# Kernel optimization log

Measured on AMD Instinct MI355X. Metric: run time of the kernel, lower is better.

The kernel has to match this reference:

```python
import jax, jax.numpy as jnp
import numpy as np

D_MODEL = 1024
D_STATE = 16
D_FFN = 4096
D_INNER = 2 * D_MODEL
DT_RANK = D_MODEL // 16  # 64
K = 3  # conv kernel size
B_SZ = 2
L = 2048


def setup_inputs() -> dict:
    key = jax.random.key(0)
    ks = jax.random.split(key, 10)
    f = jnp.float32
    s = 0.02
    A_log = jnp.log(jnp.broadcast_to(jnp.arange(1, D_STATE + 1, dtype=f), (D_INNER, D_STATE)))
    return {
        "x": jax.random.normal(ks[0], (B_SZ, L, D_MODEL), f),
        "in_proj_w": jax.random.normal(ks[1], (2 * D_INNER, D_MODEL), f) * s,
        "conv_w": jax.random.normal(ks[2], (D_INNER, K), f) * s,
        "conv_b": jnp.zeros((D_INNER,), f),
        "x_proj_w": jax.random.normal(ks[3], (DT_RANK + 2 * D_STATE, D_INNER), f) * s,
        "dt_proj_w": jax.random.normal(ks[4], (D_INNER, DT_RANK), f) * s,
        "dt_proj_b": jnp.full((D_INNER,), -4.0, f),  # softplus -> small init dt
        "A_log": A_log,
        "Dp": jnp.ones((D_INNER,), f),
        "out_proj_w": jax.random.normal(ks[5], (D_MODEL, D_INNER), f) * s,
        "w1": jax.random.normal(ks[6], (D_FFN, D_MODEL), f) * s,
        "b1": jnp.zeros((D_FFN,), f),
        "w2": jax.random.normal(ks[7], (D_MODEL, D_FFN), f) * s,
        "b2": jnp.zeros((D_MODEL,), f),
    }


def _mamba(x, in_proj_w, conv_w, conv_b, x_proj_w, dt_proj_w, dt_proj_b, A_log, Dp, out_proj_w):
    # x: [B, L, d_model]
    xz = x @ in_proj_w.T                       # [B, L, 2*d_inner]
    xp, z = jnp.split(xz, 2, axis=-1)          # each [B, L, d_inner]
    # causal depthwise conv over time
    xc = jnp.swapaxes(xp, 1, 2)                # [B, d_inner, L]
    kern = conv_w[:, None, :]                  # [d_inner, 1, K]
    xc = jax.lax.conv_general_dilated(xc, kern, (1,), [(K - 1, 0)], feature_group_count=D_INNER)
    xp = jax.nn.silu(jnp.swapaxes(xc, 1, 2) + conv_b)  # [B, L, d_inner]
    # input-dependent dt, B, C
    dbc = xp @ x_proj_w.T                      # [B, L, dt_rank + 2*d_state]
    dt = jax.nn.softplus(dbc[..., :DT_RANK] @ dt_proj_w.T + dt_proj_b)  # [B, L, d_inner]
    Bm = dbc[..., DT_RANK:DT_RANK + D_STATE]   # [B, L, d_state]
    Cm = dbc[..., DT_RANK + D_STATE:]          # [B, L, d_state]
    A = -jnp.exp(A_log)                        # [d_inner, d_state]

    def step(h, t):
        dt_t, B_t, C_t, x_t = t                # [B,d_inner],[B,n],[B,n],[B,d_inner]
        h = jnp.exp(dt_t[:, :, None] * A) * h + dt_t[:, :, None] * B_t[:, None, :] * x_t[:, :, None]
        y = jnp.einsum('bdn,bn->bd', h, C_t)
        return h, y

    h0 = jnp.zeros((x.shape[0], D_INNER, D_STATE), x.dtype)
    ts = (jnp.swapaxes(dt, 0, 1), jnp.swapaxes(Bm, 0, 1), jnp.swapaxes(Cm, 0, 1), jnp.swapaxes(xp, 0, 1))
    h_final, ys = jax.lax.scan(step, h0, ts)
    y = jnp.swapaxes(ys, 0, 1) + xp * Dp       # [B, L, d_inner]
    y = y * jax.nn.silu(z)
    return y @ out_proj_w.T, h_final


def reference(x, in_proj_w, conv_w, conv_b, x_proj_w, dt_proj_w, dt_proj_b, A_log, Dp, out_proj_w, w1, b1, w2, b2):
    ssm_out, new_state = _mamba(x, in_proj_w, conv_w, conv_b, x_proj_w, dt_proj_w, dt_proj_b, A_log, Dp, out_proj_w)
    x = x + ssm_out
    h = jax.nn.gelu(x @ w1.T + b1, approximate=False)
    x = x + (h @ w2.T + b2)
    return (x, new_state)
```

## Files before the change

### kernel.cpp

```cpp
#include <hip/hip_runtime.h>
#include <hip/hip_bf16.h>
#include <math.h>

using bf16 = __hip_bfloat16;

typedef __attribute__((ext_vector_type(8))) short short8;
typedef __attribute__((ext_vector_type(4))) short shortx4;
typedef __attribute__((ext_vector_type(4))) float floatx4;

#define D_MODEL 1024
#define D_STATE 16
#define D_FFN   4096
#define D_INNER 2048
#define DT_RANK 64
#define BSZ     2
#define SEQ     2048
#define MROWS   (BSZ*SEQ)
#define NCHUNK  16
#define CLEN    (SEQ/NCHUNK)

static __device__ __forceinline__ float bf2f(bf16 v) { return __bfloat162float(v); }
static __device__ __forceinline__ short f2s(float f) {
    bf16 h = __float2bfloat16(f);
    return *reinterpret_cast<short*>(&h);
}
static __device__ __forceinline__ float sbf(short s) {
    union { short s; bf16 h; } u; u.s = s; return __bfloat162float(u.h);
}
static __device__ __forceinline__ float rd(const bf16* p)  { return bf2f(*p); }
static __device__ __forceinline__ float rd(const float* p) { return *p; }
static __device__ __forceinline__ void  wr(bf16* p, float v)  { *p = __float2bfloat16(v); }
static __device__ __forceinline__ void  wr(float* p, float v) { *p = v; }

static __device__ __forceinline__ void gload16(const bf16* g, bf16* l) {
    __builtin_amdgcn_global_load_lds(
        (const __attribute__((address_space(1))) void*)g,
        (__attribute__((address_space(3))) void*)l, 16, 0, 0);
}

#define BK 32

enum { ACT_NONE = 0, ACT_GELU = 1, ACT_SOFTPLUS = 2 };

template<int ACT, bool HAS_BIAS, bool HAS_RES, typename TR, typename TC>
__global__ __launch_bounds__(256)
void gemm_bt(const bf16* __restrict__ A, int lda,
             const bf16* __restrict__ W,
             TC* __restrict__ C, int ldc,
             const float* __restrict__ bias,
             const TR* __restrict__ resid, int ldr,
             int K)
{
    __shared__ __align__(16) bf16 As[128 * BK];
    __shared__ __align__(16) bf16 Bs[128 * BK];

    const int tid  = threadIdx.x;
    const int lane = tid & 63;
    const int wid  = tid >> 6;
    const int wm   = wid >> 1;
    const int wn   = wid & 1;
    const int quad = lane >> 4;
    const int lrow = lane & 15;

    const long m0 = (long)blockIdx.y * 128;
    const long n0 = (long)blockIdx.x * 128;

    const int rA = lane >> 2;
    const int kA = (lane & 3) * 8;
    const int q0 = wid * 2, q1 = wid * 2 + 1;

    const bf16* Ag0 = A + (m0 + q0 * 16 + rA) * (long)lda + kA;
    const bf16* Ag1 = A + (m0 + q1 * 16 + rA) * (long)lda + kA;
    const bf16* Wg0 = W + (n0 + q0 * 16 + rA) * (long)K + kA;
    const bf16* Wg1 = W + (n0 + q1 * 16 + rA) * (long)K + kA;
    bf16* AsL0 = As + q0 * 512;
    bf16* AsL1 = As + q1 * 512;
    bf16* BsL0 = Bs + q0 * 512;
    bf16* BsL1 = Bs + q1 * 512;

    floatx4 acc[4][4] = {};

    for (int k0 = 0; k0 < K; k0 += BK) {
        __syncthreads();
        gload16(Ag0 + k0, AsL0);
        gload16(Ag1 + k0, AsL1);
        gload16(Wg0 + k0, BsL0);
        gload16(Wg1 + k0, BsL1);
        __syncthreads();

        short8 af[4], bfv[4];
        #pragma unroll
        for (int i = 0; i < 4; i++)
            af[i] = *(const short8*)(As + (wm * 64 + i * 16 + lrow) * BK + quad * 8);
        #pragma unroll
        for (int j = 0; j < 4; j++)
            bfv[j] = *(const short8*)(Bs + (wn * 64 + j * 16 + lrow) * BK + quad * 8);
        #pragma unroll
        for (int i = 0; i < 4; i++)
            #pragma unroll
            for (int j = 0; j < 4; j++)
                acc[i][j] = __builtin_amdgcn_mfma_f32_16x16x32_bf16(af[i], bfv[j], acc[i][j], 0, 0, 0);
    }

    #pragma unroll
    for (int j = 0; j < 4; j++) {
        const long col = n0 + wn * 64 + j * 16 + lrow;
        float bv = HAS_BIAS ? bias[col] : 0.0f;
        #pragma unroll
        for (int i = 0; i < 4; i++) {
            #pragma unroll
            for (int r = 0; r < 4; r++) {
                const long row = m0 + wm * 64 + i * 16 + quad * 4 + r;
                float v = acc[i][j][r] + bv;
                if (ACT == ACT_GELU)     v = 0.5f * v * (1.0f + erff(v * 0.70710678118f));
                if (ACT == ACT_SOFTPLUS) v = (v > 20.0f) ? v : log1pf(__expf(v));
                if (HAS_RES) v += rd(resid + row * (long)ldr + col);
                wr(C + row * (long)ldc + col, v);
            }
        }
    }
}

__global__ __launch_bounds__(256)
void cvt_bf16(const float* __restrict__ src, bf16* __restrict__ dst)
{
    long i = (long)blockIdx.x * 256 + threadIdx.x;
    float4 a = *((const float4*)src + i * 2);
    float4 b = *((const float4*)src + i * 2 + 1);
    short8 r;
    r[0] = f2s(a.x); r[1] = f2s(a.y); r[2] = f2s(a.z); r[3] = f2s(a.w);
    r[4] = f2s(b.x); r[5] = f2s(b.y); r[6] = f2s(b.z); r[7] = f2s(b.w);
    *(short8*)(dst + i * 8) = r;
}

__global__ __launch_bounds__(256)
void conv_silu(const bf16* __restrict__ xpre, const float* __restrict__ cw,
               const float* __restrict__ cb, bf16* __restrict__ xp)
{
    long i = (long)blockIdx.x * 256 + threadIdx.x;
    int  d  = (int)(i & (D_INNER - 1));
    long bl = i >> 11;
    long l  = bl & (SEQ - 1);

    float w0 = cw[d * 3 + 0];
    float w1 = cw[d * 3 + 1];
    float w2 = cw[d * 3 + 2];
    float acc = cb[d] + w2 * bf2f(xpre[i]);
    if (l >= 1) acc += w1 * bf2f(xpre[i - D_INNER]);
    if (l >= 2) acc += w0 * bf2f(xpre[i - 2 * D_INNER]);
    float s = acc / (1.0f + __expf(-acc));
    xp[i] = __float2bfloat16(s);
}

__global__ __launch_bounds__(256)
void pad_xproj(const float* __restrict__ src, bf16* __restrict__ dst)
{
    int i = blockIdx.x * 256 + threadIdx.x;
    int row = i >> 11, col = i & 2047;
    dst[i] = (row < 96) ? __float2bfloat16(src[row * 2048 + col])
                        : __float2bfloat16(0.0f);
}

#define SROWS 16
#define SDB   64
#define SNB   (CLEN/SROWS)

__global__ __launch_bounds__(256)
void scan_part(const bf16* __restrict__ dt, const bf16* __restrict__ xp,
               const bf16* __restrict__ dbc, const float* __restrict__ Alog,
               float* __restrict__ Pbuf, float* __restrict__ Qbuf)
{
    __shared__ float2 Ap[2][SROWS][SDB];
    __shared__ float  Bp[2][SROWS][16];

    const int tid  = threadIdx.x;
    const int c    = blockIdx.x & (NCHUNK - 1);
    const int dgrp = (blockIdx.x >> 4) & 31;
    const int b    = blockIdx.x >> 9;
    const int d0   = dgrp * SDB;
    const long row0 = (long)b * SEQ + (long)c * CLEN;

    const int sl  = tid >> 4;
    const int sq  = tid & 15;
    const int sd4 = sq * 4;

    const int nt = tid & 3;
    const int dl = tid >> 2;
    const int n0 = nt * 4;
    const int d  = d0 + dl;

    const float4 Av = *(const float4*)(Alog + d * 16 + n0);
    float Ad[4] = { -__expf(Av.x), -__expf(Av.y), -__expf(Av.z), -__expf(Av.w) };

    float rdt[4], rdx[4], rB;
    auto ldb = [&](int bb) {
        long row = row0 + bb * SROWS + sl;
        shortx4 dv = *(const shortx4*)(dt + row * D_INNER + d0 + sd4);
        shortx4 xv = *(const shortx4*)(xp + row * D_INNER + d0 + sd4);
        #pragma unroll
        for (int k = 0; k < 4; k++) {
            float f = sbf(dv[k]);
            rdt[k] = f;
            rdx[k] = f * sbf(xv[k]);
        }
        rB = bf2f(dbc[row * 128 + 64 + sq]);
    };
    auto stb = [&](int bb) {
        int s = bb & 1;
        #pragma unroll
        for (int k = 0; k < 4; k++)
            Ap[s][sl][sd4 + k] = make_float2(rdt[k], rdx[k]);
        Bp[s][sl][sq] = rB;
    };

    float h[4] = {0.f, 0.f, 0.f, 0.f};
    float sdt = 0.f;

    ldb(0); stb(0);
    for (int bb = 0; bb < SNB; bb++) {
        if (bb + 1 < SNB) ldb(bb + 1);
        __syncthreads();
        const int s = bb & 1;
        #pragma unroll
        for (int l = 0; l < SROWS; l++) {
            float2  a  = Ap[s][l][dl];
            floatx4 Bq = *(const floatx4*)&Bp[s][l][n0];
            sdt += a.x;
            #pragma unroll
            for (int k = 0; k < 4; k++)
                h[k] = __expf(a.x * Ad[k]) * h[k] + a.y * Bq[k];
        }
        if (bb + 1 < SNB) stb(bb + 1);
    }

    const long base = ((long)(b * NCHUNK + c) * D_INNER + d) * 16 + n0;
    floatx4 P = { __expf(Ad[0] * sdt), __expf(Ad[1] * sdt),
                  __expf(Ad[2] * sdt), __expf(Ad[3] * sdt) };
    floatx4 Q = { h[0], h[1], h[2], h[3] };
    *(floatx4*)(Pbuf + base) = P;
    *(floatx4*)(Qbuf + base) = Q;
}

__global__ __launch_bounds__(256)
void scan_combine(const float* __restrict__ Pbuf, float* __restrict__ Qbuf,
                  float* __restrict__ state)
{
    long i = (long)blockIdx.x * 256 + threadIdx.x;
    int  n = (int)(i & 15);
    int  d = (int)((i >> 4) & (D_INNER - 1));
    int  b = (int)(i >> 15);
    float h = 0.0f;
    #pragma unroll
    for (int c = 0; c < NCHUNK; c++) {
        const long idx = ((long)(b * NCHUNK + c) * D_INNER + d) * 16 + n;
        float P = Pbuf[idx], Q = Qbuf[idx];
        Qbuf[idx] = h;
        h = P * h + Q;
    }
    state[((long)b * D_INNER + d) * 16 + n] = h;
}

__global__ __launch_bounds__(256)
void scan_final(const bf16* __restrict__ dt, bf16* __restrict__ xp,
                const bf16* __restrict__ dbc, const float* __restrict__ Alog,
                const bf16* __restrict__ z, const float* __restrict__ Dp,
                const float* __restrict__ Qbuf)
{
    __shared__ float2 Ap [2][SROWS][SDB];
    __shared__ float2 BCp[2][SROWS][16];
    __shared__ float2 GWp[2][SROWS][SDB];

    const int tid  = threadIdx.x;
    const int c    = blockIdx.x & (NCHUNK - 1);
    const int dgrp = (blockIdx.x >> 4) & 31;
    const int b    = blockIdx.x >> 9;
    const int d0   = dgrp * SDB;
    const long row0 = (long)b * SEQ + (long)c * CLEN;

    const int sl  = tid >> 4;
    const int sq  = tid & 15;
    const int sd4 = sq * 4;

    const int nt = tid & 3;
    const int dl = tid >> 2;
    const int n0 = nt * 4;
    const int d  = d0 + dl;

    const float4 Av = *(const float4*)(Alog + d * 16 + n0);
    float Ad[4] = { -__expf(Av.x), -__expf(Av.y), -__expf(Av.z), -__expf(Av.w) };
    const float4 Dv = *(const float4*)(Dp + d0 + sd4);
    const float Dk[4] = { Dv.x, Dv.y, Dv.z, Dv.w };

    float rdt[4], rdx[4], rg[4], rw[4], rB, rC;
    auto ldb = [&](int bb) {
        long row = row0 + bb * SROWS + sl;
        shortx4 dv = *(const shortx4*)(dt + row * D_INNER + d0 + sd4);
        shortx4 xv = *(const shortx4*)(xp + row * D_INNER + d0 + sd4);
        shortx4 zv = *(const shortx4*)(z  + row * D_INNER + d0 + sd4);
        #pragma unroll
        for (int k = 0; k < 4; k++) {
            float f  = sbf(dv[k]);
            float xf = sbf(xv[k]);
            float zf = sbf(zv[k]);
            float g  = zf / (1.0f + __expf(-zf));
            rdt[k] = f;
            rdx[k] = f * xf;
            rg[k]  = g;
            rw[k]  = xf * Dk[k] * g;
        }
        rB = bf2f(dbc[row * 128 + 64 + sq]);
        rC = bf2f(dbc[row * 128 + 80 + sq]);
    };
    auto stb = [&](int bb) {
        int s = bb & 1;
        #pragma unroll
        for (int k = 0; k < 4; k++) {
            Ap [s][sl][sd4 + k] = make_float2(rdt[k], rdx[k]);
            GWp[s][sl][sd4 + k] = make_float2(rg[k], rw[k]);
        }
        BCp[s][sl][sq] = make_float2(rB, rC);
    };

    float h[4];
    {
        const long base = ((long)(b * NCHUNK + c) * D_INNER + d) * 16 + n0;
        floatx4 q = *(const floatx4*)(Qbuf + base);
        h[0] = q[0]; h[1] = q[1]; h[2] = q[2]; h[3] = q[3];
    }

    ldb(0); stb(0);
    for (int bb = 0; bb < SNB; bb++) {
        if (bb + 1 < SNB) ldb(bb + 1);
        __syncthreads();
        const int s = bb & 1;
        #pragma unroll
        for (int l = 0; l < SROWS; l++) {
            float2  a   = Ap[s][l][dl];
            floatx4 bc0 = *(const floatx4*)&BCp[s][l][n0];
            floatx4 bc1 = *(const floatx4*)&BCp[s][l][n0 + 2];
            float yv;
            h[0] = __expf(a.x * Ad[0]) * h[0] + a.y * bc0[0];
            yv   = h[0] * bc0[1];
            h[1] = __expf(a.x * Ad[1]) * h[1] + a.y * bc0[2];
            yv  += h[1] * bc0[3];
            h[2] = __expf(a.x * Ad[2]) * h[2] + a.y * bc1[0];
            yv  += h[2] * bc1[1];
            h[3] = __expf(a.x * Ad[3]) * h[3] + a.y * bc1[2];
            yv  += h[3] * bc1[3];
            yv += __shfl_xor(yv, 1);
            yv += __shfl_xor(yv, 2);
            if (nt == 0) {
                float2 gw = GWp[s][l][dl];
                float out = yv * gw.x + gw.y;
                xp[(row0 + bb * SROWS + l) * (long)D_INNER + d0 + dl] =
                    __float2bfloat16(out);
            }
        }
        if (bb + 1 < SNB) stb(bb + 1);
    }
}

extern "C" void kernel_launch(void* const* d_in, const int* in_sizes, int n_in,
                              void* d_out, int out_size, void* d_ws, size_t ws_size,
                              hipStream_t stream)
{
    const float* x      = (const float*)d_in[0];
    const float* inw    = (const float*)d_in[1];
    const float* convw  = (const float*)d_in[2];
    const float* convb  = (const float*)d_in[3];
    const float* xprojw = (const float*)d_in[4];
    const float* dtw    = (const float*)d_in[5];
    const float* dtbias = (const float*)d_in[6];
    const float* Alog   = (const float*)d_in[7];
    const float* Dp     = (const float*)d_in[8];
    const float* outw   = (const float*)d_in[9];
    const float* w1     = (const float*)d_in[10];
    const float* b1     = (const float*)d_in[11];
    const float* w2     = (const float*)d_in[12];
    const float* b2     = (const float*)d_in[13];

    float* out0 = (float*)d_out;
    float* out1 = out0 + (long)MROWS * D_MODEL;

    bf16* buf0 = (bf16*)d_ws;
    bf16* buf1 = buf0 + (long)MROWS * D_INNER;
    bf16* buf2 = buf1 + (long)MROWS * D_INNER;
    bf16* dbc  = buf2 + (long)MROWS * D_INNER;
    bf16* wpad = dbc  + (long)MROWS * 128;
    bf16* W8   = wpad + 128 * 2048;

    float* Pbuf = (float*)d_out;
    float* Qbuf = Pbuf + (long)BSZ * NCHUNK * D_INNER * 16;
    bf16*  xbf  = (bf16*)((char*)d_out + 8 * 1024 * 1024);

    dim3 blk(256);

    cvt_bf16<<<dim3(2048), blk, 0, stream>>>(x, xbf);
    cvt_bf16<<<dim3(2048), blk, 0, stream>>>(inw, W8);
    pad_xproj<<<dim3(1024), blk, 0, stream>>>(xprojw, wpad);

    gemm_bt<ACT_NONE, false, false, float, bf16>
        <<<dim3(16, 32), blk, 0, stream>>>(
        xbf, D_MODEL, W8, buf0, D_INNER, nullptr, (const float*)nullptr, 0, D_MODEL);

    gemm_bt<ACT_NONE, false, false, float, bf16>
        <<<dim3(16, 32), blk, 0, stream>>>(
        xbf, D_MODEL, W8 + (long)D_INNER * D_MODEL, buf2, D_INNER,
        nullptr, (const float*)nullptr, 0, D_MODEL);

    conv_silu<<<dim3(32768), blk, 0, stream>>>(buf0, convw, convb, buf1);

    gemm_bt<ACT_NONE, false, false, float, bf16>
        <<<dim3(1, 32), blk, 0, stream>>>(
        buf1, D_INNER, wpad, dbc, 128, nullptr, (const float*)nullptr, 0, D_INNER);

    cvt_bf16<<<dim3(64), blk, 0, stream>>>(dtw, W8);
    gemm_bt<ACT_SOFTPLUS, true, false, float, bf16>
        <<<dim3(16, 32), blk, 0, stream>>>(
        dbc, 128, W8, buf0, D_INNER, dtbias, (const float*)nullptr, 0, DT_RANK);

    scan_part<<<dim3(BSZ * NCHUNK * (D_INNER / SDB)), blk, 0, stream>>>(
        buf0, buf1, dbc, Alog, Pbuf, Qbuf);
    scan_combine<<<dim3(256), blk, 0, stream>>>(Pbuf, Qbuf, out1);
    scan_final<<<dim3(BSZ * NCHUNK * (D_INNER / SDB)), blk, 0, stream>>>(
        buf0, buf1, dbc, Alog, buf2, Dp, Qbuf);

    cvt_bf16<<<dim3(1024), blk, 0, stream>>>(outw, W8);
    gemm_bt<ACT_NONE, false, true, float, bf16>
        <<<dim3(8, 32), blk, 0, stream>>>(
        buf1, D_INNER, W8, buf2, D_MODEL, nullptr, x, D_MODEL, D_INNER);

    cvt_bf16<<<dim3(2048), blk, 0, stream>>>(w1, W8);
    gemm_bt<ACT_GELU, true, false, float, bf16>
        <<<dim3(32, 32), blk, 0, stream>>>(
        buf2, D_MODEL, W8, buf0, D_FFN, b1, (const float*)nullptr, 0, D_MODEL);

    cvt_bf16<<<dim3(2048), blk, 0, stream>>>(w2, W8);
    gemm_bt<ACT_NONE, true, true, bf16, float>
        <<<dim3(8, 32), blk, 0, stream>>>(
        buf0, D_FFN, W8, out0, D_MODEL, b2, buf2, D_MODEL, D_FFN);
}
```

Baseline: 601.4 us.

## Widen GEMM K-tile to 64 with XOR-swizzled LDS, grid remap, merged in_proj launch

Doubles the GEMM K tile to 64, so each tile load is followed by two MFMA sub-steps, and XOR-swizzles the LDS layout to avoid bank conflicts on the fragment reads. It also remaps block indices into bands for better L2 locality and merges the two in_proj GEMMs into one launch by splitting the grid across two weight/output pairs. The aim is fewer barriers per unit of work, less LDS conflict stalling and one less launch. The cost is doubled LDS use per block, which may lower occupancy, and the DT GEMM with K=64 now runs a single k-iteration.

```diff
diff --git a/kernel.cpp b/kernel.cpp
--- a/kernel.cpp
+++ b/kernel.cpp
@@ -38,18 +38,19 @@
         (__attribute__((address_space(3))) void*)l, 16, 0, 0);
 }
 
-#define BK 32
+#define BK 64
 
 enum { ACT_NONE = 0, ACT_GELU = 1, ACT_SOFTPLUS = 2 };
 
 template<int ACT, bool HAS_BIAS, bool HAS_RES, typename TR, typename TC>
 __global__ __launch_bounds__(256)
 void gemm_bt(const bf16* __restrict__ A, int lda,
-             const bf16* __restrict__ W,
+             const bf16* __restrict__ W, int ldw,
              TC* __restrict__ C, int ldc,
              const float* __restrict__ bias,
              const TR* __restrict__ resid, int ldr,
-             int K)
+             int K,
+             const bf16* __restrict__ W2, TC* __restrict__ C2, int mtiles)
 {
     __shared__ __align__(16) bf16 As[128 * BK];
     __shared__ __align__(16) bf16 Bs[128 * BK];
@@ -62,44 +63,62 @@
     const int quad = lane >> 4;
     const int lrow = lane & 15;
 
-    const long m0 = (long)blockIdx.y * 128;
-    const long n0 = (long)blockIdx.x * 128;
-
-    const int rA = lane >> 2;
-    const int kA = (lane & 3) * 8;
-    const int q0 = wid * 2, q1 = wid * 2 + 1;
-
-    const bf16* Ag0 = A + (m0 + q0 * 16 + rA) * (long)lda + kA;
-    const bf16* Ag1 = A + (m0 + q1 * 16 + rA) * (long)lda + kA;
-    const bf16* Wg0 = W + (n0 + q0 * 16 + rA) * (long)K + kA;
-    const bf16* Wg1 = W + (n0 + q1 * 16 + rA) * (long)K + kA;
-    bf16* AsL0 = As + q0 * 512;
-    bf16* AsL1 = As + q1 * 512;
-    bf16* BsL0 = Bs + q0 * 512;
-    bf16* BsL1 = Bs + q1 * 512;
+    int bx = blockIdx.x, by = blockIdx.y;
+    const int gx = gridDim.x;
+    if ((gx & 7) == 0) {
+        int id = by * gx + bx;
+        int bw = gx >> 3;
+        int band = id & 7, s = id >> 3;
+        bx = band * bw + (s % bw);
+        by = s / bw;
+    }
+    if (by >= mtiles) { by -= mtiles; W = W2; C = C2; }
+
+    const long m0 = (long)by * 128;
+    const long n0 = (long)bx * 128;
+
+    const int rsub = lane >> 3;
+    const int k8   = (lane & 7) ^ rsub;
+    const int g0   = wid * 4;
+
+    const bf16* Ag[4]; const bf16* Wg[4];
+    #pragma unroll
+    for (int j = 0; j < 4; j++) {
+        Ag[j] = A + (m0 + 8 * (g0 + j) + rsub) * (long)lda + k8 * 8;
+        Wg[j] = W + (n0 + 8 * (g0 + j) + rsub) * (long)ldw + k8 * 8;
+    }
+
+    const int xorl  = lrow & 7;
+    const int coK0  = ((quad)     ^ xorl) * 8;
+    const int coK1  = ((quad + 4) ^ xorl) * 8;
 
     floatx4 acc[4][4] = {};
 
     for (int k0 = 0; k0 < K; k0 += BK) {
         __syncthreads();
-        gload16(Ag0 + k0, AsL0);
-        gload16(Ag1 + k0, AsL1);
-        gload16(Wg0 + k0, BsL0);
-        gload16(Wg1 + k0, BsL1);
+        #pragma unroll
+        for (int j = 0; j < 4; j++) {
+            gload16(Ag[j] + k0, As + (g0 + j) * 512);
+            gload16(Wg[j] + k0, Bs + (g0 + j) * 512);
+        }
         __syncthreads();
 
-        short8 af[4], bfv[4];
-        #pragma unroll
-        for (int i = 0; i < 4; i++)
-            af[i] = *(const short8*)(As + (wm * 64 + i * 16 + lrow) * BK + quad * 8);
-        #pragma unroll
-        for (int j = 0; j < 4; j++)
-            bfv[j] = *(const short8*)(Bs + (wn * 64 + j * 16 + lrow) * BK + quad * 8);
-        #pragma unroll
-        for (int i = 0; i < 4; i++)
+        #pragma unroll
+        for (int kk = 0; kk < 2; kk++) {
+            const int co = kk ? coK1 : coK0;
+            short8 af[4], bfv[4];
+            #pragma unroll
+            for (int i = 0; i < 4; i++)
+                af[i] = *(const short8*)(As + (wm * 64 + i * 16 + lrow) * BK + co);
             #pragma unroll
             for (int j = 0; j < 4; j++)
-                acc[i][j] = __builtin_amdgcn_mfma_f32_16x16x32_bf16(af[i], bfv[j], acc[i][j], 0, 0, 0);
+                bfv[j] = *(const short8*)(Bs + (wn * 64 + j * 16 + lrow) * BK + co);
+            #pragma unroll
+            for (int i = 0; i < 4; i++)
+                #pragma unroll
+                for (int j = 0; j < 4; j++)
+                    acc[i][j] = __builtin_amdgcn_mfma_f32_16x16x32_bf16(af[i], bfv[j], acc[i][j], 0, 0, 0);
+        }
     }
 
     #pragma unroll
@@ -394,30 +413,29 @@
     bf16*  xbf  = (bf16*)((char*)d_out + 8 * 1024 * 1024);
 
     dim3 blk(256);
+    const float* nf = nullptr;
 
     cvt_bf16<<<dim3(2048), blk, 0, stream>>>(x, xbf);
     cvt_bf16<<<dim3(2048), blk, 0, stream>>>(inw, W8);
     pad_xproj<<<dim3(1024), blk, 0, stream>>>(xprojw, wpad);
 
     gemm_bt<ACT_NONE, false, false, float, bf16>
-        <<<dim3(16, 32), blk, 0, stream>>>(
-        xbf, D_MODEL, W8, buf0, D_INNER, nullptr, (const float*)nullptr, 0, D_MODEL);
-
-    gemm_bt<ACT_NONE, false, false, float, bf16>
-        <<<dim3(16, 32), blk, 0, stream>>>(
-        xbf, D_MODEL, W8 + (long)D_INNER * D_MODEL, buf2, D_INNER,
-        nullptr, (const float*)nullptr, 0, D_MODEL);
+        <<<dim3(16, 64), blk, 0, stream>>>(
+        xbf, D_MODEL, W8, D_MODEL, buf0, D_INNER, nullptr, nf, 0, D_MODEL,
+        W8 + (long)D_INNER * D_MODEL, buf2, 32);
 
     conv_silu<<<dim3(32768), blk, 0, stream>>>(buf0, convw, convb, buf1);
 
     gemm_bt<ACT_NONE, false, false, float, bf16>
         <<<dim3(1, 32), blk, 0, stream>>>(
-        buf1, D_INNER, wpad, dbc, 128, nullptr, (const float*)nullptr, 0, D_INNER);
+        buf1, D_INNER, wpad, D_INNER, dbc, 128, nullptr, nf, 0, D_INNER,
+        wpad, dbc, 1000);
 
     cvt_bf16<<<dim3(64), blk, 0, stream>>>(dtw, W8);
     gemm_bt<ACT_SOFTPLUS, true, false, float, bf16>
         <<<dim3(16, 32), blk, 0, stream>>>(
-        dbc, 128, W8, buf0, D_INNER, dtbias, (const float*)nullptr, 0, DT_RANK);
+        dbc, 128, W8, DT_RANK, buf0, D_INNER, dtbias, nf, 0, DT_RANK,
+        W8, buf0, 1000);
 
     scan_part<<<dim3(BSZ * NCHUNK * (D_INNER / SDB)), blk, 0, stream>>>(
         buf0, buf1, dbc, Alog, Pbuf, Qbuf);
@@ -428,15 +446,18 @@
     cvt_bf16<<<dim3(1024), blk, 0, stream>>>(outw, W8);
     gemm_bt<ACT_NONE, false, true, float, bf16>
         <<<dim3(8, 32), blk, 0, stream>>>(
-        buf1, D_INNER, W8, buf2, D_MODEL, nullptr, x, D_MODEL, D_INNER);
+        buf1, D_INNER, W8, D_INNER, buf2, D_MODEL, nullptr, x, D_MODEL, D_INNER,
+        W8, buf2, 1000);
 
     cvt_bf16<<<dim3(2048), blk, 0, stream>>>(w1, W8);
     gemm_bt<ACT_GELU, true, false, float, bf16>
         <<<dim3(32, 32), blk, 0, stream>>>(
-        buf2, D_MODEL, W8, buf0, D_FFN, b1, (const float*)nullptr, 0, D_MODEL);
+        buf2, D_MODEL, W8, D_MODEL, buf0, D_FFN, b1, nf, 0, D_MODEL,
+        W8, buf0, 1000);
 
     cvt_bf16<<<dim3(2048), blk, 0, stream>>>(w2, W8);
     gemm_bt<ACT_NONE, true, true, bf16, float>
         <<<dim3(8, 32), blk, 0, stream>>>(
-        buf0, D_FFN, W8, out0, D_MODEL, b2, buf2, D_MODEL, D_FFN);
-}
+        buf0, D_FFN, W8, D_FFN, out0, D_MODEL, b2, buf2, D_MODEL, D_FFN,
+        W8, out0, 1000);
+}
```

Result: faster. 570.3 us (-5.2%).
